# Performance work log

Measured on AMD Instinct MI355X. Metric: run time of the kernel, lower is better.

The kernel has to match this reference:

```python
import jax, jax.numpy as jnp
import numpy as np
from jax import lax

B, L, D, H, N, V, K = 2, 1024, 512, 8, 4, 32000, 64
HD = D // H


def layer_norm(x, g, b, eps=1e-5):
    m = jnp.mean(x, axis=-1, keepdims=True)
    v = jnp.var(x, axis=-1, keepdims=True)
    return (x - m) * lax.rsqrt(v + eps) * g + b


def setup_inputs() -> dict:
    ks = jax.random.split(jax.random.key(0), 16)
    s = 0.02
    return {
        "x_q": jax.random.normal(ks[0], (B, L, D), jnp.float32),
        "x": jax.random.randint(ks[1], (B, L), 0, V, jnp.int32),
        "E_slots": jax.random.normal(ks[2], (V, D), jnp.float32),
        "rhos": jax.random.uniform(ks[3], (N,), jnp.float32, 0.9, 0.999),
        "C_seq": jax.random.uniform(ks[4], (B, L, N), jnp.float32),
        "c_base": jax.random.uniform(ks[5], (B, K, N), jnp.float32),
        "unique_slots": jax.random.randint(ks[6], (B, K), 0, V, jnp.int32),
        "pad_mask": jnp.ones((B, K), jnp.bool_),
        "Wq": jax.random.normal(ks[7], (D, D), jnp.float32) * s,
        "Wk": jax.random.normal(ks[8], (D, D), jnp.float32) * s,
        "Wv": jax.random.normal(ks[9], (D, D), jnp.float32) * s,
        "Wo": jax.random.normal(ks[10], (D, D), jnp.float32) * s,
        "W_pe": jax.random.normal(ks[11], (N, D), jnp.float32) * s,
        "ln_kv_g": jnp.ones((D,), jnp.float32),
        "ln_kv_b": jnp.zeros((D,), jnp.float32),
        "ln_q_g": jnp.ones((D,), jnp.float32),
        "ln_q_b": jnp.zeros((D,), jnp.float32),
    }


def reference(x_q, x, E_slots, rhos, C_seq, c_base, unique_slots, pad_mask,
              Wq, Wk, Wv, Wo, W_pe, ln_kv_g, ln_kv_b, ln_q_g, ln_q_b):
    # --- projections (dropout is eval-mode identity) ---
    memory_base = layer_norm(E_slots, ln_kv_g, ln_kv_b)          # [V,D]
    E_k = (memory_base @ Wk).reshape(V, H, HD)                   # [V,H,hd]
    E_v = (memory_base @ Wv).reshape(V, H, HD)
    P_gate = (C_seq + 1.0) @ W_pe                                # [B,L,D]
    Q = layer_norm(x_q * P_gate, ln_q_g, ln_q_b) @ Wq            # [B,L,D]

    # --- initial EMA state from history ---
    safe = jnp.maximum(unique_slots, 0)                          # [B,K]
    ek0 = E_k[safe]                                              # [B,K,H,hd]
    ev0 = E_v[safe]
    outer0 = ek0[..., :, None] * ev0[..., None, :]               # [B,K,H,hd,hd]
    cb = c_base * pad_mask[..., None].astype(c_base.dtype)
    S0 = jnp.einsum('bkn,bkhij->bhnij', cb, outer0).astype(jnp.float32)  # [B,H,N,hd,hd]

    W_pe_hn = W_pe.reshape(N, H, HD).transpose(1, 0, 2)          # [H,N,hd]
    rhos_b = rhos[None, None, :, None, None]

    Qh = Q.reshape(B, L, H, HD).transpose(1, 0, 2, 3)            # [L,B,H,hd]
    toks = x.T                                                   # [L,B]

    def step(S, inp):
        q_t, tok = inp                                           # [B,H,hd], [B]
        S = S * rhos_b                                           # decay
        q_mod = q_t[:, :, None, :] * W_pe_hn[None]               # [B,H,N,hd]
        o_t = jnp.einsum('bhnd,bhnde->bhe', q_mod, S)            # sum over n, contract d
        ek_t = E_k[tok]                                          # [B,H,hd]
        ev_t = E_v[tok]
        outer = ek_t[..., :, None] * ev_t[..., None, :]          # [B,H,hd,hd]
        S = S + outer[:, :, None]                                # broadcast over N
        return S, o_t

    _, O = lax.scan(step, S0, (Qh, toks))                        # O: [L,B,H,hd]
    O = O.transpose(1, 0, 2, 3).reshape(B, L, D)
    return O @ Wo
```

## Files before the change

### kernel.cpp

```cpp
#include <hip/hip_runtime.h>

namespace {

constexpr int B = 2, L = 1024, D = 512, H = 8, N = 4, KSL = 64;
constexpr int CHK = 64;
constexpr int NCK = L / CHK;
constexpr int ROWS = B * L + B * KSL;

static_assert(D == 512 && N == 4, "layout assumptions");

typedef _Float16 half8 __attribute__((ext_vector_type(8)));
typedef _Float16 half4v __attribute__((ext_vector_type(4)));
typedef _Float16 half2t __attribute__((ext_vector_type(2)));
typedef float f32x4 __attribute__((ext_vector_type(4)));

__global__ __launch_bounds__(256) void k_pre(
    const float* __restrict__ Wk, const float* __restrict__ Wv,
    const float* __restrict__ Wq, const float* __restrict__ Wo,
    _Float16* __restrict__ WTh,
    const float* __restrict__ E_slots, const int* __restrict__ x,
    const int* __restrict__ uniq, const float* __restrict__ kv_g,
    const float* __restrict__ kv_b, _Float16* __restrict__ lnEh,
    const float* __restrict__ x_q, const float* __restrict__ C_seq,
    const float* __restrict__ W_pe, const float* __restrict__ q_g,
    const float* __restrict__ q_b, _Float16* __restrict__ lnqh) {
  __shared__ _Float16 trh[64 * 66];
  __shared__ float red[8];
  int bid = blockIdx.x;
  int t = threadIdx.x;

  if (bid < 256) {
    int widx = bid >> 6, tile = bid & 63;
    int k0 = (tile >> 3) * 64, n0 = (tile & 7) * 64;
    const float* W = widx == 0 ? Wk : widx == 1 ? Wv : widx == 2 ? Wq : Wo;
#pragma unroll
    for (int i = 0; i < 16; ++i) {
      int idx = t + i * 256, r = idx >> 6, c = idx & 63;
      trh[c * 66 + r] = (_Float16)W[(size_t)(k0 + r) * 512 + n0 + c];
    }
    __syncthreads();
    _Float16* WT = WTh + (size_t)widx * 512 * 512;
#pragma unroll
    for (int i = 0; i < 8; ++i) {
      int idx = t + i * 256, rr = idx >> 5, cc = (idx & 31) * 2;
      half2t v = {trh[rr * 66 + cc], trh[rr * 66 + cc + 1]};
      *(half2t*)&WT[(size_t)(n0 + rr) * 512 + k0 + cc] = v;
    }
    return;
  }

  float vx, vy;
  const float* g;
  const float* bb;
  _Float16* dst;
  int d0 = t * 2;
  if (bid < 256 + ROWS) {
    int r = bid - 256;
    int idx;
    if (r < B * L) {
      idx = x[r];
    } else {
      int u = uniq[r - B * L];
      idx = u > 0 ? u : 0;
    }
    float2 v = *(const float2*)(E_slots + (size_t)idx * D + d0);
    vx = v.x;
    vy = v.y;
    g = kv_g; bb = kv_b;
    dst = lnEh + (size_t)r * D + d0;
  } else {
    int r = bid - 256 - ROWS;
    float c0 = C_seq[r * 4 + 0] + 1.f;
    float c1 = C_seq[r * 4 + 1] + 1.f;
    float c2 = C_seq[r * 4 + 2] + 1.f;
    float c3 = C_seq[r * 4 + 3] + 1.f;
    float p0 = c0 * W_pe[d0] + c1 * W_pe[512 + d0] + c2 * W_pe[1024 + d0] + c3 * W_pe[1536 + d0];
    float p1 = c0 * W_pe[d0 + 1] + c1 * W_pe[513 + d0] + c2 * W_pe[1025 + d0] + c3 * W_pe[1537 + d0];
    float2 xv = *(const float2*)(x_q + (size_t)r * D + d0);
    vx = xv.x * p0;
    vy = xv.y * p1;
    g = q_g; bb = q_b;
    dst = lnqh + (size_t)r * D + d0;
  }
  float s = vx + vy;
  float s2 = vx * vx + vy * vy;
#pragma unroll
  for (int o = 32; o > 0; o >>= 1) {
    s += __shfl_down(s, o);
    s2 += __shfl_down(s2, o);
  }
  if ((t & 63) == 0) {
    red[(t >> 6) * 2] = s;
    red[(t >> 6) * 2 + 1] = s2;
  }
  __syncthreads();
  float S = red[0] + red[2] + red[4] + red[6];
  float S2 = red[1] + red[3] + red[5] + red[7];
  float m = S * (1.f / D);
  float inv = rsqrtf(S2 * (1.f / D) - m * m + 1e-5f);
  half2t o2;
  o2.x = (_Float16)((vx - m) * inv * g[d0] + bb[d0]);
  o2.y = (_Float16)((vy - m) * inv * g[d0 + 1] + bb[d0 + 1]);
  *(half2t*)dst = o2;
}

__global__ __launch_bounds__(512) void k_gemm3(
    const _Float16* __restrict__ A0, const _Float16* __restrict__ Wt0, _Float16* __restrict__ C0, int M0,
    const _Float16* __restrict__ A1, const _Float16* __restrict__ Wt1, _Float16* __restrict__ C1, int M1,
    const _Float16* __restrict__ A2, const _Float16* __restrict__ Wt2, _Float16* __restrict__ C2, int M2) {
  const _Float16* A;
  const _Float16* Wt;
  _Float16* C;
  int M;
  int z = blockIdx.z;
  if (z == 0) { A = A0; Wt = Wt0; C = C0; M = M0; }
  else if (z == 1) { A = A1; Wt = Wt1; C = C1; M = M1; }
  else { A = A2; Wt = Wt2; C = C2; M = M2; }
  int m0 = blockIdx.y * 128;
  if (m0 >= M) return;
  int n0 = blockIdx.x * 128;

  constexpr int LDA = 40;
  __shared__ _Float16 As[128 * LDA];
  __shared__ _Float16 Ws[128 * LDA];

  int t = threadIdx.x;
  int lane = t & 63, w = t >> 6;
  int wr = (w >> 1) * 32, wc = (w & 1) * 64;
  int fr = lane & 15, kg = (lane >> 4) * 8;
  int srow = t >> 2, sseg = (t & 3) * 8;

  f32x4 zero4 = {0.f, 0.f, 0.f, 0.f};
  f32x4 acc[2][4];
#pragma unroll
  for (int i = 0; i < 2; ++i)
#pragma unroll
    for (int j = 0; j < 4; ++j) acc[i][j] = zero4;

  for (int k0 = 0; k0 < 512; k0 += 32) {
    half8 av = *(const half8*)(A + (size_t)(m0 + srow) * 512 + k0 + sseg);
    half8 wv = *(const half8*)(Wt + (size_t)(n0 + srow) * 512 + k0 + sseg);
    __syncthreads();
    *(half8*)&As[srow * LDA + sseg] = av;
    *(half8*)&Ws[srow * LDA + sseg] = wv;
    __syncthreads();
    half8 af[2], bf[4];
#pragma unroll
    for (int mt = 0; mt < 2; ++mt) af[mt] = *(half8*)&As[(wr + mt * 16 + fr) * LDA + kg];
#pragma unroll
    for (int nt = 0; nt < 4; ++nt) bf[nt] = *(half8*)&Ws[(wc + nt * 16 + fr) * LDA + kg];
#pragma unroll
    for (int mt = 0; mt < 2; ++mt)
#pragma unroll
      for (int nt = 0; nt < 4; ++nt)
        acc[mt][nt] = __builtin_amdgcn_mfma_f32_16x16x32_f16(af[mt], bf[nt], acc[mt][nt], 0, 0, 0);
  }
  int crow = (lane >> 4) * 4, ccol = lane & 15;
#pragma unroll
  for (int mt = 0; mt < 2; ++mt)
#pragma unroll
    for (int nt = 0; nt < 4; ++nt)
#pragma unroll
      for (int r = 0; r < 4; ++r)
        C[(size_t)(m0 + wr + mt * 16 + crow + r) * 512 + n0 + wc + nt * 16 + ccol] =
            (_Float16)acc[mt][nt][r];
}

__global__ __launch_bounds__(256) void k_gemm64(const _Float16* __restrict__ A,
                                                const _Float16* __restrict__ Wt,
                                                float* __restrict__ C) {
  int m0 = blockIdx.y * 64, n0 = blockIdx.x * 64;
  constexpr int LDA = 40;
  __shared__ _Float16 As[64 * LDA];
  __shared__ _Float16 Ws[64 * LDA];
  int t = threadIdx.x;
  int lane = t & 63, w = t >> 6;
  int wr = (w >> 1) * 32, wc = (w & 1) * 32;
  int fr = lane & 15, kg = (lane >> 4) * 8;
  bool isA = t < 128;
  int li = t & 127;
  int row = li >> 1, seg = (li & 1) * 16;
  const _Float16* src = isA ? A + (size_t)(m0 + row) * 512 + seg
                            : Wt + (size_t)(n0 + row) * 512 + seg;
  _Float16* dst = (isA ? As : Ws) + row * LDA + seg;

  f32x4 zero4 = {0.f, 0.f, 0.f, 0.f};
  f32x4 acc[2][2];
#pragma unroll
  for (int i = 0; i < 2; ++i)
#pragma unroll
    for (int j = 0; j < 2; ++j) acc[i][j] = zero4;

  for (int k0 = 0; k0 < 512; k0 += 32) {
    half8 a0 = *(const half8*)(src + k0);
    half8 a1 = *(const half8*)(src + k0 + 8);
    __syncthreads();
    *(half8*)dst = a0;
    *(half8*)(dst + 8) = a1;
    __syncthreads();
    half8 af[2], bf[2];
#pragma unroll
    for (int mt = 0; mt < 2; ++mt) af[mt] = *(half8*)&As[(wr + mt * 16 + fr) * LDA + kg];
#pragma unroll
    for (int nt = 0; nt < 2; ++nt) bf[nt] = *(half8*)&Ws[(wc + nt * 16 + fr) * LDA + kg];
#pragma unroll
    for (int mt = 0; mt < 2; ++mt)
#pragma unroll
      for (int nt = 0; nt < 2; ++nt)
        acc[mt][nt] = __builtin_amdgcn_mfma_f32_16x16x32_f16(af[mt], bf[nt], acc[mt][nt], 0, 0, 0);
  }
  int crow = (lane >> 4) * 4, ccol = lane & 15;
#pragma unroll
  for (int mt = 0; mt < 2; ++mt)
#pragma unroll
    for (int nt = 0; nt < 2; ++nt)
#pragma unroll
      for (int r = 0; r < 4; ++r)
        C[(size_t)(m0 + wr + mt * 16 + crow + r) * 512 + n0 + wc + nt * 16 + ccol] =
            acc[mt][nt][r];
}

__global__ __launch_bounds__(256) void k_dct(const _Float16* __restrict__ EKh,
                                             const _Float16* __restrict__ EVh,
                                             const float* __restrict__ rhos,
                                             const float* __restrict__ c_base,
                                             _Float16* __restrict__ DCt,
                                             _Float16* __restrict__ S0t) {
  constexpr int LDH = 72;
  __shared__ _Float16 ekt[64 * LDH];
  __shared__ _Float16 evt[64 * LDH];
  __shared__ float cb[64][4];
  __shared__ float rls4[4];
  int bid = blockIdx.x;
  int t = threadIdx.x;
  bool is_s0 = bid >= B * H * NCK;
  int row = t >> 2, seg = (t & 3) * 16;
  size_t grow;
  if (!is_s0) {
    int c = bid % NCK, h = (bid / NCK) % H, b = bid / (NCK * H);
    grow = (size_t)(b * L + c * CHK + row) * 512 + h * 64 + seg;
  } else {
    int bh = bid - B * H * NCK;
    int h = bh % H, b = bh / H;
    grow = (size_t)(B * L + b * KSL + row) * 512 + h * 64 + seg;
    int uu = t >> 2, nn = t & 3;
    cb[uu][nn] = c_base[(b * KSL + uu) * N + nn];
  }
  half8 e0 = *(const half8*)(EKh + grow);
  half8 e1 = *(const half8*)(EKh + grow + 8);
  half8 v0 = *(const half8*)(EVh + grow);
  half8 v1 = *(const half8*)(EVh + grow + 8);
#pragma unroll
  for (int i = 0; i < 8; ++i) {
    ekt[(seg + i) * LDH + row] = e0[i];
    ekt[(seg + 8 + i) * LDH + row] = e1[i];
    evt[(seg + i) * LDH + row] = v0[i];
    evt[(seg + 8 + i) * LDH + row] = v1[i];
  }
  if (t < 4) rls4[t] = log2f(rhos[t]);
  __syncthreads();

  int lane = t & 63, w = t >> 6;
  int wr = (w >> 1) * 32, wc = (w & 1) * 32;
  int fr = lane & 15, kg = (lane >> 4) * 8;
  int crow = (lane >> 4) * 4, ccol = lane & 15;

  half8 ef[2][2], bf[2][2];
#pragma unroll
  for (int mt = 0; mt < 2; ++mt)
#pragma unroll
    for (int ks = 0; ks < 2; ++ks)
      ef[mt][ks] = *(const half8*)&evt[(wr + mt * 16 + fr) * LDH + ks * 32 + kg];
#pragma unroll
  for (int nt = 0; nt < 2; ++nt)
#pragma unroll
    for (int ks = 0; ks < 2; ++ks)
      bf[nt][ks] = *(const half8*)&ekt[(wc + nt * 16 + fr) * LDH + ks * 32 + kg];

  f32x4 zero4 = {0.f, 0.f, 0.f, 0.f};
#pragma unroll
  for (int n = 0; n < 4; ++n) {
    half8 dec0, dec1;
    if (!is_s0) {
      float l2r = rls4[n];
#pragma unroll
      for (int i = 0; i < 8; ++i) {
        dec0[i] = (_Float16)exp2f((float)(CHK - (kg + i)) * l2r);
        dec1[i] = (_Float16)exp2f((float)(CHK - (32 + kg + i)) * l2r);
      }
    } else {
#pragma unroll
      for (int i = 0; i < 8; ++i) {
        dec0[i] = (_Float16)cb[kg + i][n];
        dec1[i] = (_Float16)cb[32 + kg + i][n];
      }
    }
    half8 af0a = ef[0][0] * dec0, af0b = ef[0][1] * dec1;
    half8 af1a = ef[1][0] * dec0, af1b = ef[1][1] * dec1;
    f32x4 acc[2][2];
#pragma unroll
    for (int i = 0; i < 2; ++i)
#pragma unroll
      for (int j = 0; j < 2; ++j) acc[i][j] = zero4;
#pragma unroll
    for (int nt = 0; nt < 2; ++nt) {
      acc[0][nt] = __builtin_amdgcn_mfma_f32_16x16x32_f16(af0a, bf[nt][0], acc[0][nt], 0, 0, 0);
      acc[0][nt] = __builtin_amdgcn_mfma_f32_16x16x32_f16(af0b, bf[nt][1], acc[0][nt], 0, 0, 0);
      acc[1][nt] = __builtin_amdgcn_mfma_f32_16x16x32_f16(af1a, bf[nt][0], acc[1][nt], 0, 0, 0);
      acc[1][nt] = __builtin_amdgcn_mfma_f32_16x16x32_f16(af1b, bf[nt][1], acc[1][nt], 0, 0, 0);
    }
    _Float16* dp = is_s0 ? S0t + ((size_t)(bid - B * H * NCK) * N + n) * 4096
                         : DCt + ((size_t)bid * N + n) * 4096;
#pragma unroll
    for (int mt = 0; mt < 2; ++mt)
#pragma unroll
      for (int nt = 0; nt < 2; ++nt)
#pragma unroll
        for (int r = 0; r < 4; ++r)
          dp[(wr + mt * 16 + crow + r) * 64 + wc + nt * 16 + ccol] = (_Float16)acc[mt][nt][r];
  }
}

__global__ void k_gscan(const _Float16* __restrict__ S0t, const _Float16* __restrict__ DCt,
                        const float* __restrict__ rhos, _Float16* __restrict__ GT) {
  int bhn = blockIdx.x >> 2, sl = blockIdx.x & 3;
  int n = bhn % N, bh = bhn / N;
  float rho = rhos[n];
  float rhoC = exp2f(64.f * log2f(rho));
  int off = sl * 1024 + threadIdx.x * 4;
  float gv[4];
  {
    half4v a = *(const half4v*)(S0t + (size_t)bhn * 4096 + off);
#pragma unroll
    for (int i = 0; i < 4; ++i) gv[i] = rho * (float)a[i];
  }
  _Float16* gp = GT + (size_t)bhn * NCK * 4096 + off;
  half4v cur = *(const half4v*)(DCt + ((size_t)(bh * NCK) * N + n) * 4096 + off);
  for (int cc = 0; cc < NCK; ++cc) {
    half4v o;
#pragma unroll
    for (int i = 0; i < 4; ++i) o[i] = (_Float16)gv[i];
    *(half4v*)(gp + (size_t)cc * 4096) = o;
    if (cc + 1 < NCK) {
      half4v nx = *(const half4v*)(DCt + ((size_t)(bh * NCK + cc + 1) * N + n) * 4096 + off);
#pragma unroll
      for (int i = 0; i < 4; ++i) gv[i] = rhoC * gv[i] + (float)cur[i];
      cur = nx;
    }
  }
}

__global__ __launch_bounds__(256) void k_chunk(
    const _Float16* __restrict__ Qh, const _Float16* __restrict__ EKh,
    const _Float16* __restrict__ EVh, const _Float16* __restrict__ GT,
    const float* __restrict__ W_pe, const float* __restrict__ rhos,
    _Float16* __restrict__ OAh) {
  int bid = blockIdx.x;
  int c = bid % NCK, h = (bid / NCK) % H, b = bid / (NCK * H);
  constexpr int LDH = 72;
  __shared__ _Float16 qs[64 * LDH];
  __shared__ _Float16 eks[64 * LDH];
  __shared__ _Float16 evt[64 * LDH];
  __shared__ _Float16 gts[4][64 * LDH];
  __shared__ _Float16 wsm[64 * LDH];
  __shared__ float wpe[4][64];
  __shared__ float rls[4];
  int t = threadIdx.x;
  {
    int row = t >> 2, seg = (t & 3) * 16;
    size_t grow = (size_t)(b * L + c * CHK + row) * 512 + h * 64 + seg;
    half8 q0 = *(const half8*)(Qh + grow);
    half8 q1 = *(const half8*)(Qh + grow + 8);
    half8 k0 = *(const half8*)(EKh + grow);
    half8 k1 = *(const half8*)(EKh + grow + 8);
    half8 v0 = *(const half8*)(EVh + grow);
    half8 v1 = *(const half8*)(EVh + grow + 8);
    *(half8*)&qs[row * LDH + seg] = q0;
    *(half8*)&qs[row * LDH + seg + 8] = q1;
    *(half8*)&eks[row * LDH + seg] = k0;
    *(half8*)&eks[row * LDH + seg + 8] = k1;
#pragma unroll
    for (int i = 0; i < 8; ++i) {
      evt[(seg + i) * LDH + row] = v0[i];
      evt[(seg + 8 + i) * LDH + row] = v1[i];
    }
#pragma unroll
    for (int n = 0; n < 4; ++n) {
      const _Float16* gpp = GT + (((size_t)(b * H + h) * N + n) * NCK + c) * 4096 + row * 64 + seg;
      *(half8*)&gts[n][row * LDH + seg] = *(const half8*)gpp;
      *(half8*)&gts[n][row * LDH + seg + 8] = *(const half8*)(gpp + 8);
    }
    int nn = t >> 6, dd = t & 63;
    wpe[nn][dd] = W_pe[nn * 512 + h * 64 + dd];
    if (t < 4) rls[t] = log2f(rhos[t]);
  }
  __syncthreads();

  int lane = t & 63, w = t >> 6;
  int u0 = w * 16;
  int fr = lane & 15, kg = (lane >> 4) * 8;
  int crow = (lane >> 4) * 4, ccol = lane & 15;

  half8 qf0 = *(const half8*)&qs[(u0 + fr) * LDH + kg];
  half8 qf1 = *(const half8*)&qs[(u0 + fr) * LDH + 32 + kg];

  f32x4 zero4 = {0.f, 0.f, 0.f, 0.f};
  f32x4 oa[4], wacc[4];
#pragma unroll
  for (int i = 0; i < 4; ++i) { oa[i] = zero4; wacc[i] = zero4; }

#pragma unroll
  for (int n = 0; n < 4; ++n) {
    float l2r = rls[n];
    half8 am0, am1;
#pragma unroll
    for (int i = 0; i < 8; ++i) {
      am0[i] = (_Float16)((float)qf0[i] * wpe[n][kg + i]);
      am1[i] = (_Float16)((float)qf1[i] * wpe[n][32 + kg + i]);
    }
    float ru[4];
#pragma unroll
    for (int r = 0; r < 4; ++r) ru[r] = exp2f((float)(u0 + crow + r) * l2r);
#pragma unroll
    for (int et = 0; et < 4; ++et) {
      f32x4 ta = zero4;
      ta = __builtin_amdgcn_mfma_f32_16x16x32_f16(
          am0, *(const half8*)&gts[n][(et * 16 + fr) * LDH + kg], ta, 0, 0, 0);
      ta = __builtin_amdgcn_mfma_f32_16x16x32_f16(
          am1, *(const half8*)&gts[n][(et * 16 + fr) * LDH + 32 + kg], ta, 0, 0, 0);
#pragma unroll
      for (int r = 0; r < 4; ++r) oa[et][r] += ru[r] * ta[r];
    }
#pragma unroll
    for (int vt = 0; vt < 4; ++vt) {
      f32x4 sa = zero4;
      sa = __builtin_amdgcn_mfma_f32_16x16x32_f16(
          am0, *(const half8*)&eks[(vt * 16 + fr) * LDH + kg], sa, 0, 0, 0);
      sa = __builtin_amdgcn_mfma_f32_16x16x32_f16(
          am1, *(const half8*)&eks[(vt * 16 + fr) * LDH + 32 + kg], sa, 0, 0, 0);
      float rv = exp2f(-(float)(vt * 16 + ccol) * l2r);
      int v = vt * 16 + ccol;
#pragma unroll
      for (int r = 0; r < 4; ++r) {
        int u = u0 + crow + r;
        float coef = (v < u) ? ru[r] * rv : 0.f;
        wacc[vt][r] += coef * sa[r];
      }
    }
  }
#pragma unroll
  for (int vt = 0; vt < 4; ++vt)
#pragma unroll
    for (int r = 0; r < 4; ++r)
      wsm[(u0 + crow + r) * LDH + vt * 16 + ccol] = (_Float16)wacc[vt][r];
  half8 wf0 = *(const half8*)&wsm[(u0 + fr) * LDH + kg];
  half8 wf1 = *(const half8*)&wsm[(u0 + fr) * LDH + 32 + kg];
#pragma unroll
  for (int et = 0; et < 4; ++et) {
    oa[et] = __builtin_amdgcn_mfma_f32_16x16x32_f16(
        wf0, *(const half8*)&evt[(et * 16 + fr) * LDH + kg], oa[et], 0, 0, 0);
    oa[et] = __builtin_amdgcn_mfma_f32_16x16x32_f16(
        wf1, *(const half8*)&evt[(et * 16 + fr) * LDH + 32 + kg], oa[et], 0, 0, 0);
  }
#pragma unroll
  for (int et = 0; et < 4; ++et)
#pragma unroll
    for (int r = 0; r < 4; ++r)
      OAh[(size_t)(b * L + c * CHK + u0 + crow + r) * 512 + h * 64 + et * 16 + ccol] =
          (_Float16)oa[et][r];
}

}

extern "C" void kernel_launch(void* const* d_in, const int* in_sizes, int n_in,
                              void* d_out, int out_size, void* d_ws, size_t ws_size,
                              hipStream_t stream) {
  const float* x_q = (const float*)d_in[0];
  const int* x = (const int*)d_in[1];
  const float* E_slots = (const float*)d_in[2];
  const float* rhos = (const float*)d_in[3];
  const float* C_seq = (const float*)d_in[4];
  const float* c_base = (const float*)d_in[5];
  const int* uniq = (const int*)d_in[6];
  const float* Wq = (const float*)d_in[8];
  const float* Wk = (const float*)d_in[9];
  const float* Wv = (const float*)d_in[10];
  const float* Wo = (const float*)d_in[11];
  const float* W_pe = (const float*)d_in[12];
  const float* ln_kv_g = (const float*)d_in[13];
  const float* ln_kv_b = (const float*)d_in[14];
  const float* ln_q_g = (const float*)d_in[15];
  const float* ln_q_b = (const float*)d_in[16];
  float* out = (float*)d_out;

  _Float16* hb = (_Float16*)d_ws;
  _Float16* lnEh = hb;
  _Float16* lnqh = lnEh + 1114112;
  _Float16* WTh = lnqh + 1048576;
  _Float16* EKh = WTh + 1048576;
  _Float16* EVh = EKh + 1114112;
  _Float16* Qh = EVh + 1114112;
  _Float16* DCt = Qh + 1048576;
  _Float16* S0t = DCt + 4194304;
  _Float16* GT = S0t + 262144;
  _Float16* OAh = GT + 4194304;

  const _Float16* WTk = WTh;
  const _Float16* WTv = WTh + 262144;
  const _Float16* WTq = WTh + 524288;
  const _Float16* WTo = WTh + 786432;

  k_pre<<<256 + ROWS + B * L, 256, 0, stream>>>(
      Wk, Wv, Wq, Wo, WTh, E_slots, x, uniq, ln_kv_g, ln_kv_b, lnEh,
      x_q, C_seq, W_pe, ln_q_g, ln_q_b, lnqh);
  k_gemm3<<<dim3(4, 17, 3), 512, 0, stream>>>(lnEh, WTk, EKh, ROWS,
                                              lnEh, WTv, EVh, ROWS,
                                              lnqh, WTq, Qh, B * L);
  k_dct<<<B * H * NCK + B * H, 256, 0, stream>>>(EKh, EVh, rhos, c_base, DCt, S0t);
  k_gscan<<<B * H * N * 4, 256, 0, stream>>>(S0t, DCt, rhos, GT);
  k_chunk<<<B * H * NCK, 256, 0, stream>>>(Qh, EKh, EVh, GT, W_pe, rhos, OAh);
  k_gemm64<<<dim3(8, 32), 256, 0, stream>>>(OAh, WTo, out);
}
```

Before: 47.84 us.

## Double-buffer GEMMs with direct global-to-LDS loads and precompute decay tables

Both projection GEMMs now use global_load_lds to copy tiles straight into double-buffered, XOR-swizzled shared memory with a K-step of 64, so the next tile is prefetched during the MFMAs and there is one barrier per step instead of two. The chunk kernels replace per-thread exp2f decay computation with small shared-memory tables (decay powers, c_base, and fp16 W_pe), and the prefix-scan kernel prefetches two chunks ahead. This cuts global-load latency stalls and transcendental work but doubles LDS use in the GEMMs and adds fp16 rounding on the W_pe product.

```diff
diff --git a/kernel.cpp b/kernel.cpp
--- a/kernel.cpp
+++ b/kernel.cpp
@@ -1,4 +1,5 @@
 #include <hip/hip_runtime.h>
+#include <stdint.h>
 
 namespace {
 
@@ -13,6 +14,12 @@
 typedef _Float16 half4v __attribute__((ext_vector_type(4)));
 typedef _Float16 half2t __attribute__((ext_vector_type(2)));
 typedef float f32x4 __attribute__((ext_vector_type(4)));
+
+__device__ __forceinline__ void gld16(_Float16* lds_dst, const _Float16* gsrc) {
+  __builtin_amdgcn_global_load_lds(
+      (const __attribute__((address_space(1))) unsigned int*)gsrc,
+      (__attribute__((address_space(3))) unsigned int*)lds_dst, 16, 0, 0);
+}
 
 __global__ __launch_bounds__(256) void k_pre(
     const float* __restrict__ Wk, const float* __restrict__ Wv,
@@ -120,15 +127,22 @@
   if (m0 >= M) return;
   int n0 = blockIdx.x * 128;
 
-  constexpr int LDA = 40;
-  __shared__ _Float16 As[128 * LDA];
-  __shared__ _Float16 Ws[128 * LDA];
+  __shared__ _Float16 As[2][128 * 64];
+  __shared__ _Float16 Ws[2][128 * 64];
 
   int t = threadIdx.x;
   int lane = t & 63, w = t >> 6;
   int wr = (w >> 1) * 32, wc = (w & 1) * 64;
   int fr = lane & 15, kg = (lane >> 4) * 8;
-  int srow = t >> 2, sseg = (t & 3) * 8;
+  int kq = kg >> 3, fx = fr & 7;
+  int pA = kq ^ fx, pB = (4 + kq) ^ fx;
+
+  int srow = t >> 3;
+  int sseg = ((t & 7) ^ (srow & 7)) * 8;
+  int wbase = w * 512;
+
+  const _Float16* gA = A + (size_t)(m0 + srow) * 512 + sseg;
+  const _Float16* gB = Wt + (size_t)(n0 + srow) * 512 + sseg;
 
   f32x4 zero4 = {0.f, 0.f, 0.f, 0.f};
   f32x4 acc[2][4];
@@ -137,23 +151,43 @@
 #pragma unroll
     for (int j = 0; j < 4; ++j) acc[i][j] = zero4;
 
-  for (int k0 = 0; k0 < 512; k0 += 32) {
-    half8 av = *(const half8*)(A + (size_t)(m0 + srow) * 512 + k0 + sseg);
-    half8 wv = *(const half8*)(Wt + (size_t)(n0 + srow) * 512 + k0 + sseg);
-    __syncthreads();
-    *(half8*)&As[srow * LDA + sseg] = av;
-    *(half8*)&Ws[srow * LDA + sseg] = wv;
-    __syncthreads();
-    half8 af[2], bf[4];
-#pragma unroll
-    for (int mt = 0; mt < 2; ++mt) af[mt] = *(half8*)&As[(wr + mt * 16 + fr) * LDA + kg];
-#pragma unroll
-    for (int nt = 0; nt < 4; ++nt) bf[nt] = *(half8*)&Ws[(wc + nt * 16 + fr) * LDA + kg];
+  gld16(&As[0][wbase], gA);
+  gld16(&As[0][wbase + 4096], gA + 64 * 512);
+  gld16(&Ws[0][wbase], gB);
+  gld16(&Ws[0][wbase + 4096], gB + 64 * 512);
+  __syncthreads();
+
+  int buf = 0;
+  for (int s8 = 0; s8 < 8; ++s8) {
+    if (s8 < 7) {
+      int k0 = (s8 + 1) * 64;
+      gld16(&As[buf ^ 1][wbase], gA + k0);
+      gld16(&As[buf ^ 1][wbase + 4096], gA + 64 * 512 + k0);
+      gld16(&Ws[buf ^ 1][wbase], gB + k0);
+      gld16(&Ws[buf ^ 1][wbase + 4096], gB + 64 * 512 + k0);
+    }
+    half8 af[2][2], bf[4][2];
+#pragma unroll
+    for (int mt = 0; mt < 2; ++mt) {
+      int row = wr + mt * 16 + fr;
+      af[mt][0] = *(const half8*)&As[buf][row * 64 + pA * 8];
+      af[mt][1] = *(const half8*)&As[buf][row * 64 + pB * 8];
+    }
+#pragma unroll
+    for (int nt = 0; nt < 4; ++nt) {
+      int row = wc + nt * 16 + fr;
+      bf[nt][0] = *(const half8*)&Ws[buf][row * 64 + pA * 8];
+      bf[nt][1] = *(const half8*)&Ws[buf][row * 64 + pB * 8];
+    }
 #pragma unroll
     for (int mt = 0; mt < 2; ++mt)
 #pragma unroll
-      for (int nt = 0; nt < 4; ++nt)
-        acc[mt][nt] = __builtin_amdgcn_mfma_f32_16x16x32_f16(af[mt], bf[nt], acc[mt][nt], 0, 0, 0);
+      for (int nt = 0; nt < 4; ++nt) {
+        acc[mt][nt] = __builtin_amdgcn_mfma_f32_16x16x32_f16(af[mt][0], bf[nt][0], acc[mt][nt], 0, 0, 0);
+        acc[mt][nt] = __builtin_amdgcn_mfma_f32_16x16x32_f16(af[mt][1], bf[nt][1], acc[mt][nt], 0, 0, 0);
+      }
+    if (s8 < 7) __syncthreads();
+    buf ^= 1;
   }
   int crow = (lane >> 4) * 4, ccol = lane & 15;
 #pragma unroll
@@ -170,19 +204,21 @@
                                                 const _Float16* __restrict__ Wt,
                                                 float* __restrict__ C) {
   int m0 = blockIdx.y * 64, n0 = blockIdx.x * 64;
-  constexpr int LDA = 40;
-  __shared__ _Float16 As[64 * LDA];
-  __shared__ _Float16 Ws[64 * LDA];
+  __shared__ _Float16 As[2][64 * 64];
+  __shared__ _Float16 Ws[2][64 * 64];
   int t = threadIdx.x;
   int lane = t & 63, w = t >> 6;
   int wr = (w >> 1) * 32, wc = (w & 1) * 32;
   int fr = lane & 15, kg = (lane >> 4) * 8;
-  bool isA = t < 128;
-  int li = t & 127;
-  int row = li >> 1, seg = (li & 1) * 16;
-  const _Float16* src = isA ? A + (size_t)(m0 + row) * 512 + seg
-                            : Wt + (size_t)(n0 + row) * 512 + seg;
-  _Float16* dst = (isA ? As : Ws) + row * LDA + seg;
+  int kq = kg >> 3, fx = fr & 7;
+  int pA = kq ^ fx, pB = (4 + kq) ^ fx;
+
+  int srow = t >> 3;
+  int sseg = ((t & 7) ^ (srow & 7)) * 8;
+  int wbase = w * 512;
+
+  const _Float16* gA = A + (size_t)(m0 + srow) * 512 + sseg;
+  const _Float16* gB = Wt + (size_t)(n0 + srow) * 512 + sseg;
 
   f32x4 zero4 = {0.f, 0.f, 0.f, 0.f};
   f32x4 acc[2][2];
@@ -191,23 +227,43 @@
 #pragma unroll
     for (int j = 0; j < 2; ++j) acc[i][j] = zero4;
 
-  for (int k0 = 0; k0 < 512; k0 += 32) {
-    half8 a0 = *(const half8*)(src + k0);
-    half8 a1 = *(const half8*)(src + k0 + 8);
-    __syncthreads();
-    *(half8*)dst = a0;
-    *(half8*)(dst + 8) = a1;
-    __syncthreads();
-    half8 af[2], bf[2];
-#pragma unroll
-    for (int mt = 0; mt < 2; ++mt) af[mt] = *(half8*)&As[(wr + mt * 16 + fr) * LDA + kg];
-#pragma unroll
-    for (int nt = 0; nt < 2; ++nt) bf[nt] = *(half8*)&Ws[(wc + nt * 16 + fr) * LDA + kg];
+  gld16(&As[0][wbase], gA);
+  gld16(&As[0][wbase + 2048], gA + 32 * 512);
+  gld16(&Ws[0][wbase], gB);
+  gld16(&Ws[0][wbase + 2048], gB + 32 * 512);
+  __syncthreads();
+
+  int buf = 0;
+  for (int s8 = 0; s8 < 8; ++s8) {
+    if (s8 < 7) {
+      int k0 = (s8 + 1) * 64;
+      gld16(&As[buf ^ 1][wbase], gA + k0);
+      gld16(&As[buf ^ 1][wbase + 2048], gA + 32 * 512 + k0);
+      gld16(&Ws[buf ^ 1][wbase], gB + k0);
+      gld16(&Ws[buf ^ 1][wbase + 2048], gB + 32 * 512 + k0);
+    }
+    half8 af[2][2], bf[2][2];
+#pragma unroll
+    for (int mt = 0; mt < 2; ++mt) {
+      int row = wr + mt * 16 + fr;
+      af[mt][0] = *(const half8*)&As[buf][row * 64 + pA * 8];
+      af[mt][1] = *(const half8*)&As[buf][row * 64 + pB * 8];
+    }
+#pragma unroll
+    for (int nt = 0; nt < 2; ++nt) {
+      int row = wc + nt * 16 + fr;
+      bf[nt][0] = *(const half8*)&Ws[buf][row * 64 + pA * 8];
+      bf[nt][1] = *(const half8*)&Ws[buf][row * 64 + pB * 8];
+    }
 #pragma unroll
     for (int mt = 0; mt < 2; ++mt)
 #pragma unroll
-      for (int nt = 0; nt < 2; ++nt)
-        acc[mt][nt] = __builtin_amdgcn_mfma_f32_16x16x32_f16(af[mt], bf[nt], acc[mt][nt], 0, 0, 0);
+      for (int nt = 0; nt < 2; ++nt) {
+        acc[mt][nt] = __builtin_amdgcn_mfma_f32_16x16x32_f16(af[mt][0], bf[nt][0], acc[mt][nt], 0, 0, 0);
+        acc[mt][nt] = __builtin_amdgcn_mfma_f32_16x16x32_f16(af[mt][1], bf[nt][1], acc[mt][nt], 0, 0, 0);
+      }
+    if (s8 < 7) __syncthreads();
+    buf ^= 1;
   }
   int crow = (lane >> 4) * 4, ccol = lane & 15;
 #pragma unroll
@@ -229,8 +285,7 @@
   constexpr int LDH = 72;
   __shared__ _Float16 ekt[64 * LDH];
   __shared__ _Float16 evt[64 * LDH];
-  __shared__ float cb[64][4];
-  __shared__ float rls4[4];
+  __shared__ _Float16 dtab[4][64];
   int bid = blockIdx.x;
   int t = threadIdx.x;
   bool is_s0 = bid >= B * H * NCK;
@@ -239,12 +294,14 @@
   if (!is_s0) {
     int c = bid % NCK, h = (bid / NCK) % H, b = bid / (NCK * H);
     grow = (size_t)(b * L + c * CHK + row) * 512 + h * 64 + seg;
+    int nn = t >> 6, uu = t & 63;
+    dtab[nn][uu] = (_Float16)exp2f((float)(CHK - uu) * log2f(rhos[nn]));
   } else {
     int bh = bid - B * H * NCK;
     int h = bh % H, b = bh / H;
     grow = (size_t)(B * L + b * KSL + row) * 512 + h * 64 + seg;
-    int uu = t >> 2, nn = t & 3;
-    cb[uu][nn] = c_base[(b * KSL + uu) * N + nn];
+    int nn = t >> 6, uu = t & 63;
+    dtab[nn][uu] = (_Float16)c_base[(b * KSL + uu) * N + nn];
   }
   half8 e0 = *(const half8*)(EKh + grow);
   half8 e1 = *(const half8*)(EKh + grow + 8);
@@ -257,7 +314,6 @@
     evt[(seg + i) * LDH + row] = v0[i];
     evt[(seg + 8 + i) * LDH + row] = v1[i];
   }
-  if (t < 4) rls4[t] = log2f(rhos[t]);
   __syncthreads();
 
   int lane = t & 63, w = t >> 6;
@@ -280,21 +336,8 @@
   f32x4 zero4 = {0.f, 0.f, 0.f, 0.f};
 #pragma unroll
   for (int n = 0; n < 4; ++n) {
-    half8 dec0, dec1;
-    if (!is_s0) {
-      float l2r = rls4[n];
-#pragma unroll
-      for (int i = 0; i < 8; ++i) {
-        dec0[i] = (_Float16)exp2f((float)(CHK - (kg + i)) * l2r);
-        dec1[i] = (_Float16)exp2f((float)(CHK - (32 + kg + i)) * l2r);
-      }
-    } else {
-#pragma unroll
-      for (int i = 0; i < 8; ++i) {
-        dec0[i] = (_Float16)cb[kg + i][n];
-        dec1[i] = (_Float16)cb[32 + kg + i][n];
-      }
-    }
+    half8 dec0 = *(const half8*)&dtab[n][kg];
+    half8 dec1 = *(const half8*)&dtab[n][32 + kg];
     half8 af0a = ef[0][0] * dec0, af0b = ef[0][1] * dec1;
     half8 af1a = ef[1][0] * dec0, af1b = ef[1][1] * dec1;
     f32x4 acc[2][2];
@@ -336,16 +379,20 @@
   }
   _Float16* gp = GT + (size_t)bhn * NCK * 4096 + off;
   half4v cur = *(const half4v*)(DCt + ((size_t)(bh * NCK) * N + n) * 4096 + off);
+  half4v nx = *(const half4v*)(DCt + ((size_t)(bh * NCK + 1) * N + n) * 4096 + off);
   for (int cc = 0; cc < NCK; ++cc) {
     half4v o;
 #pragma unroll
     for (int i = 0; i < 4; ++i) o[i] = (_Float16)gv[i];
     *(half4v*)(gp + (size_t)cc * 4096) = o;
     if (cc + 1 < NCK) {
-      half4v nx = *(const half4v*)(DCt + ((size_t)(bh * NCK + cc + 1) * N + n) * 4096 + off);
+      half4v nx2 = cur;
+      if (cc + 2 < NCK)
+        nx2 = *(const half4v*)(DCt + ((size_t)(bh * NCK + cc + 2) * N + n) * 4096 + off);
 #pragma unroll
       for (int i = 0; i < 4; ++i) gv[i] = rhoC * gv[i] + (float)cur[i];
       cur = nx;
+      nx = nx2;
     }
   }
 }
@@ -363,8 +410,9 @@
   __shared__ _Float16 evt[64 * LDH];
   __shared__ _Float16 gts[4][64 * LDH];
   __shared__ _Float16 wsm[64 * LDH];
-  __shared__ float wpe[4][64];
-  __shared__ float rls[4];
+  __shared__ _Float16 wpeh[4][64];
+  __shared__ float rup[4][64];
+  __shared__ float rvi[4][64];
   int t = threadIdx.x;
   {
     int row = t >> 2, seg = (t & 3) * 16;
@@ -391,8 +439,10 @@
       *(half8*)&gts[n][row * LDH + seg + 8] = *(const half8*)(gpp + 8);
     }
     int nn = t >> 6, dd = t & 63;
-    wpe[nn][dd] = W_pe[nn * 512 + h * 64 + dd];
-    if (t < 4) rls[t] = log2f(rhos[t]);
+    float l2r = log2f(rhos[nn]);
+    wpeh[nn][dd] = (_Float16)W_pe[nn * 512 + h * 64 + dd];
+    rup[nn][dd] = exp2f((float)dd * l2r);
+    rvi[nn][dd] = exp2f(-(float)dd * l2r);
   }
   __syncthreads();
 
@@ -411,16 +461,11 @@
 
 #pragma unroll
   for (int n = 0; n < 4; ++n) {
-    float l2r = rls[n];
-    half8 am0, am1;
-#pragma unroll
-    for (int i = 0; i < 8; ++i) {
-      am0[i] = (_Float16)((float)qf0[i] * wpe[n][kg + i]);
-      am1[i] = (_Float16)((float)qf1[i] * wpe[n][32 + kg + i]);
-    }
+    half8 am0 = qf0 * (*(const half8*)&wpeh[n][kg]);
+    half8 am1 = qf1 * (*(const half8*)&wpeh[n][32 + kg]);
     float ru[4];
 #pragma unroll
-    for (int r = 0; r < 4; ++r) ru[r] = exp2f((float)(u0 + crow + r) * l2r);
+    for (int r = 0; r < 4; ++r) ru[r] = rup[n][u0 + crow + r];
 #pragma unroll
     for (int et = 0; et < 4; ++et) {
       f32x4 ta = zero4;
@@ -438,8 +483,8 @@
           am0, *(const half8*)&eks[(vt * 16 + fr) * LDH + kg], sa, 0, 0, 0);
       sa = __builtin_amdgcn_mfma_f32_16x16x32_f16(
           am1, *(const half8*)&eks[(vt * 16 + fr) * LDH + 32 + kg], sa, 0, 0, 0);
-      float rv = exp2f(-(float)(vt * 16 + ccol) * l2r);
       int v = vt * 16 + ccol;
+      float rv = rvi[n][v];
 #pragma unroll
       for (int r = 0; r < 4; ++r) {
         int u = u0 + crow + r;
```

After: 44.87 us. 6.2% less time.
